# Kernel tuning notes

Measured on AMD Instinct MI355X. Metric: run time of the kernel, lower is better.

## Reference

```python
import jax, jax.numpy as jnp
import numpy as np

N = 50000      # nodes
E = 800000     # edges
F_IN = 512     # num_features
H = 128        # hidden


def setup_inputs() -> dict:
    key = jax.random.key(0)
    ks = jax.random.split(key, 10)
    edge_index = jax.random.randint(ks[0], (2, E), 0, N, dtype=jnp.int64 if jax.config.jax_enable_x64 else jnp.int32)
    x = jax.random.normal(ks[1], (N, F_IN), jnp.float32)
    weights = jax.random.uniform(ks[2], (E,), jnp.float32)
    def w(i, shape, fan):
        return jax.random.normal(ks[i], shape, jnp.float32) / np.sqrt(fan).astype(np.float32)
    return {
        "edge_index": edge_index,
        "x": x,
        "weights": weights,
        "W_lin1": w(3, (F_IN, H), F_IN), "b_lin1": jnp.zeros((H,), jnp.float32),
        "W_conv1": w(4, (H, 2 * H), H), "b_conv1": jnp.zeros((2 * H,), jnp.float32),
        "W_mu": w(5, (2 * H, H), 2 * H), "b_mu": jnp.zeros((H,), jnp.float32),
        "W_lin": w(6, (2 * H, 1), 2 * H), "b_lin": jnp.zeros((1,), jnp.float32),
    }


def gcn_conv(x, W, b, src, dst, ew, n):
    """PyG GCNConv with edge weights: add self-loops (weight 1), symmetric norm, scatter-add."""
    loop = jnp.arange(n, dtype=src.dtype)
    s2 = jnp.concatenate([src, loop])
    d2 = jnp.concatenate([dst, loop])
    w2 = jnp.concatenate([ew, jnp.ones((n,), x.dtype)])
    deg = jax.ops.segment_sum(w2, d2, num_segments=n)          # weighted in-degree incl. self-loop
    dinv = jnp.where(deg > 0, deg, 1.0) ** -0.5
    dinv = jnp.where(deg > 0, dinv, 0.0)
    norm = dinv[s2] * w2 * dinv[d2]                            # [E+N]
    h = x @ W                                                   # [N, out]
    out = jax.ops.segment_sum(h[s2] * norm[:, None], d2, num_segments=n)
    return out + b


def reference(edge_index, x, weights, W_lin1, b_lin1, W_conv1, b_conv1, W_mu, b_mu, W_lin, b_lin):
    n = x.shape[0]
    src, dst = edge_index[0], edge_index[1]
    # eval mode: dropout is identity, VGAE.encode returns mu
    h = x @ W_lin1 + b_lin1                                     # lin1
    h = jax.nn.relu(gcn_conv(h, W_conv1, b_conv1, src, dst, weights, n))
    z = gcn_conv(h, W_mu, b_mu, src, dst, weights, n)           # mu == embeddings
    emb_edges = jnp.concatenate([z[src], z[dst]], axis=1)       # [E, 2H]
    out = jax.nn.sigmoid(emb_edges @ W_lin + b_lin)
    return out.squeeze(-1)                                      # [E]
```

## Files before the change

### kernel.cpp

```cpp
#include <hip/hip_runtime.h>
#include <hip/hip_bf16.h>
#include <math.h>


#define NSL 256
#define RSH 8
#define RNG 256

typedef __attribute__((ext_vector_type(8))) short bf16x8;
typedef __attribute__((ext_vector_type(4))) float f32x4;

typedef const __attribute__((address_space(1))) unsigned int* gas_t;
typedef __attribute__((address_space(3))) unsigned int* las_t;

static __device__ __forceinline__ void gload_lds16(const void* g, void* l) {
    __builtin_amdgcn_global_load_lds((gas_t)g, (las_t)l, 16, 0, 0);
}

static __device__ __forceinline__ ushort f2b(float f) {
    __hip_bfloat16 h = __float2bfloat16(f);
    return *(ushort*)&h;
}
static __device__ __forceinline__ float b2f(ushort u) {
    unsigned int v = ((unsigned int)u) << 16;
    return *(float*)&v;
}
static __device__ __forceinline__ bf16x8 cvt8(float4 a, float4 b) {
    bf16x8 r;
    r[0] = (short)f2b(a.x); r[1] = (short)f2b(a.y); r[2] = (short)f2b(a.z); r[3] = (short)f2b(a.w);
    r[4] = (short)f2b(b.x); r[5] = (short)f2b(b.y); r[6] = (short)f2b(b.z); r[7] = (short)f2b(b.w);
    return r;
}


__global__ __launch_bounds__(256) void bucket_count(const int* __restrict__ dst,
                                                    int* __restrict__ cntA, int E, int NR) {
    __shared__ int lc[256];
    const int b = blockIdx.x, t = threadIdx.x;
    lc[t] = 0;
    __syncthreads();
    const int beg = (int)((long long)b * E / NSL);
    const int end = (int)((long long)(b + 1) * E / NSL);
    for (int e = beg + t; e < end; e += 256) atomicAdd(&lc[dst[e] >> RSH], 1);
    __syncthreads();
    if (t < NR) cntA[b * NR + t] = lc[t];
}

__global__ __launch_bounds__(256) void range_scan(int* __restrict__ cntA,
                                                  int* __restrict__ rtot, int NR) {
    __shared__ int s_[256];
    const int r = blockIdx.x, t = threadIdx.x;
    int v = cntA[t * NR + r];
    s_[t] = v;
    __syncthreads();
    for (int off = 1; off < 256; off <<= 1) {
        int add = (t >= off) ? s_[t - off] : 0;
        __syncthreads();
        s_[t] += add;
        __syncthreads();
    }
    cntA[t * NR + r] = s_[t] - v;
    if (t == 255) rtot[r] = s_[t];
}

__global__ __launch_bounds__(256) void base_scan(const int* __restrict__ rtot,
                                                 int* __restrict__ baseOut, int NR) {
    __shared__ int s_[256];
    const int t = threadIdx.x;
    int v = (t < NR) ? rtot[t] : 0;
    s_[t] = v;
    __syncthreads();
    for (int off = 1; off < 256; off <<= 1) {
        int add = (t >= off) ? s_[t - off] : 0;
        __syncthreads();
        s_[t] += add;
        __syncthreads();
    }
    if (t < NR) baseOut[t] = s_[t] - v;
    if (t == NR - 1) baseOut[NR] = s_[t];
}

__global__ __launch_bounds__(256) void bucket_scatter(const int* __restrict__ src,
                                                      const int* __restrict__ dst,
                                                      const float* __restrict__ w,
                                                      const int* __restrict__ cntA,
                                                      const int* __restrict__ baseOut,
                                                      uint2* __restrict__ rec, int E, int NR) {
    __shared__ int cur[256];
    const int b = blockIdx.x, t = threadIdx.x;
    if (t < NR) cur[t] = cntA[b * NR + t] + baseOut[t];
    __syncthreads();
    const int beg = (int)((long long)b * E / NSL);
    const int end = (int)((long long)(b + 1) * E / NSL);
    for (int e = beg + t; e < end; e += 256) {
        int d = dst[e];
        int r = d >> RSH;
        int pos = atomicAdd(&cur[r], 1);
        rec[pos] = make_uint2(((unsigned int)(d & (RNG - 1)) << 24) | (unsigned int)src[e],
                              __float_as_uint(w[e]));
    }
}

__global__ __launch_bounds__(256) void range_build(const uint2* __restrict__ rec,
                                                   const int* __restrict__ baseOut,
                                                   float* __restrict__ dinv,
                                                   int* __restrict__ offs,
                                                   uint2* __restrict__ ce,
                                                   int N, int E) {
    __shared__ float lw[256];
    __shared__ int lc[256];
    __shared__ int sc[256];
    const int r = blockIdx.x, t = threadIdx.x;
    lw[t] = 0.f; lc[t] = 0;
    __syncthreads();
    const int beg = baseOut[r], end = baseOut[r + 1];
    for (int e = beg + t; e < end; e += 256) {
        uint2 pk = rec[e];
        int dl = pk.x >> 24;
        atomicAdd(&lc[dl], 1);
        atomicAdd(&lw[dl], __uint_as_float(pk.y));
    }
    __syncthreads();
    int v = lc[t];
    sc[t] = v;
    __syncthreads();
    for (int off = 1; off < 256; off <<= 1) {
        int add = (t >= off) ? sc[t - off] : 0;
        __syncthreads();
        sc[t] += add;
        __syncthreads();
    }
    const int node = (r << RSH) + t;
    const int o = beg + sc[t] - v;
    if (node < N) {
        dinv[node] = 1.0f / sqrtf(1.0f + lw[t]);
        offs[node] = o;
    }
    if (r == 0 && t == 0) offs[N] = E;
    lc[t] = o;
    __syncthreads();
    for (int e = beg + t; e < end; e += 256) {
        uint2 pk = rec[e];
        int dl = pk.x >> 24;
        int pos = atomicAdd(&lc[dl], 1);
        ce[pos] = make_uint2(pk.x & 0xFFFFFF, pk.y);
    }
}


__global__ __launch_bounds__(256) void tconv_kernel(const float* __restrict__ B,
                                                    ushort* __restrict__ BT, int K, int Nn) {
    int i = blockIdx.x * 256 + threadIdx.x;
    if (i < K * Nn) {
        int k = i / Nn, n = i % Nn;
        BT[(size_t)n * K + k] = f2b(B[i]);
    }
}

__global__ __launch_bounds__(256) void fold_kernel(const float* __restrict__ Wm,
                                                   const float* __restrict__ Wl,
                                                   const float* __restrict__ bm,
                                                   float* __restrict__ wmp,
                                                   float* __restrict__ wmq,
                                                   float* __restrict__ bpq) {
    int j = threadIdx.x;
    float sp = 0.f, sq = 0.f;
    for (int k = 0; k < 128; ++k) {
        float v = Wm[(size_t)j * 128 + k];
        sp += v * Wl[k];
        sq += v * Wl[128 + k];
    }
    wmp[j] = sp; wmq[j] = sq;
    if (j == 0) { float s = 0.f; for (int k = 0; k < 128; ++k) s += bm[k] * Wl[k];       bpq[0] = s; }
    if (j == 1) { float s = 0.f; for (int k = 0; k < 128; ++k) s += bm[k] * Wl[128 + k]; bpq[1] = s; }
}

__global__ __launch_bounds__(256) void gemm1_mfma(const float* __restrict__ A,
                                                  const ushort* __restrict__ BT,
                                                  const float* __restrict__ bias,
                                                  const float* __restrict__ dinv,
                                                  ushort* __restrict__ C, int M) {
    __shared__ float  As[2][64 * 64];
    __shared__ ushort Bs[2][128 * 64];
    const int t = threadIdx.x;
    const int bm = blockIdx.x * 64;
    const int lane = t & 63;
    const int wid = t >> 6;
    const int wm = (wid >> 1) * 32, wn = (wid & 1) * 64;

    f32x4 acc[2][4] = {};

    const int a_row_l = (lane >> 4);
    const int a_ib    = (lane & 15) * 16;
    const int b_row_l = (lane >> 3);
    const int b_ib    = (lane & 7) * 16;

    auto stage = [&](int buf, int k0) {
#pragma unroll
        for (int j = 0; j < 4; ++j) {
            int c = wid * 4 + j;
            int row = c * 4 + a_row_l;
            int sw = a_ib ^ ((row & 7) << 5);
            int grow = min(bm + row, M - 1);
            const char* src = (const char*)A + ((size_t)grow * 512 + k0) * 4 + sw;
            gload_lds16(src, (char*)As[buf] + c * 1024);
        }
#pragma unroll
        for (int j = 0; j < 4; ++j) {
            int c = wid * 4 + j;
            int row = c * 8 + b_row_l;
            int sw = b_ib ^ ((row & 7) << 4);
            const char* src = (const char*)BT + (size_t)row * 1024 + k0 * 2 + sw;
            gload_lds16(src, (char*)Bs[buf] + c * 1024);
        }
    };

    stage(0, 0);
    int cur = 0;
#pragma unroll 1
    for (int tt = 0; tt < 8; ++tt) {
        if (tt < 7) {
            stage(cur ^ 1, (tt + 1) * 64);
            asm volatile("s_waitcnt vmcnt(8)" ::: "memory");
        } else {
            asm volatile("s_waitcnt vmcnt(0)" ::: "memory");
        }
        __builtin_amdgcn_sched_barrier(0);
        __builtin_amdgcn_s_barrier();
        const char* AsB = (const char*)As[cur];
        const char* BsB = (const char*)Bs[cur];
#pragma unroll
        for (int ks = 0; ks < 2; ++ks) {
            bf16x8 af[2], bfr[4];
#pragma unroll
            for (int mi = 0; mi < 2; ++mi) {
                int r = wm + mi * 16 + (lane & 15);
                int byte = r * 256 + ks * 128 + (lane >> 4) * 32;
                byte ^= (r & 7) << 5;
                float4 f0 = *(const float4*)(AsB + byte);
                float4 f1 = *(const float4*)(AsB + byte + 16);
                af[mi] = cvt8(f0, f1);
            }
#pragma unroll
            for (int ni = 0; ni < 4; ++ni) {
                int r = wn + ni * 16 + (lane & 15);
                int byte = r * 128 + ks * 64 + (lane >> 4) * 16;
                byte ^= (r & 7) << 4;
                bfr[ni] = *(const bf16x8*)(BsB + byte);
            }
#pragma unroll
            for (int mi = 0; mi < 2; ++mi)
#pragma unroll
                for (int ni = 0; ni < 4; ++ni)
                    acc[mi][ni] = __builtin_amdgcn_mfma_f32_16x16x32_bf16(af[mi], bfr[ni], acc[mi][ni], 0, 0, 0);
        }
        __builtin_amdgcn_s_barrier();
        cur ^= 1;
    }

#pragma unroll
    for (int mi = 0; mi < 2; ++mi)
#pragma unroll
        for (int r = 0; r < 4; ++r) {
            int row = bm + wm + mi * 16 + (lane >> 4) * 4 + r;
            if (row < M) {
                float dv = dinv[row];
#pragma unroll
                for (int ni = 0; ni < 4; ++ni) {
                    int col = wn + ni * 16 + (lane & 15);
                    C[(size_t)row * 128 + col] = f2b((acc[mi][ni][r] + bias[col]) * dv);
                }
            }
        }
}

__global__ __launch_bounds__(256) void aggregate_bf16(const ushort* __restrict__ hs,
                                                      const int* __restrict__ offs,
                                                      const uint2* __restrict__ ce,
                                                      const float* __restrict__ dinv,
                                                      ushort* __restrict__ out, int n) {
    int node = (int)((blockIdx.x * (size_t)blockDim.x + threadIdx.x) >> 6);
    int lane = threadIdx.x & 63;
    if (node >= n) return;
    unsigned int hv = *(const unsigned int*)(hs + (size_t)node * 128 + lane * 2);
    float ax = b2f((ushort)(hv & 0xffff));
    float ay = b2f((ushort)(hv >> 16));
    int beg = offs[node], end = offs[node + 1];
    for (int e = beg; e < end; e += 8) {
        uint2 rr[8];
#pragma unroll
        for (int j = 0; j < 8; ++j) {
            bool v = (e + j) < end;
            rr[j] = v ? ce[e + j] : make_uint2((unsigned)node, 0u);
        }
        unsigned int vv[8];
#pragma unroll
        for (int j = 0; j < 8; ++j)
            vv[j] = *(const unsigned int*)(hs + (size_t)rr[j].x * 128 + lane * 2);
#pragma unroll
        for (int j = 0; j < 8; ++j) {
            float wj = __uint_as_float(rr[j].y);
            ax += wj * b2f((ushort)(vv[j] & 0xffff));
            ay += wj * b2f((ushort)(vv[j] >> 16));
        }
    }
    float dv = dinv[node];
    unsigned int o = (unsigned int)f2b(ax * dv) | ((unsigned int)f2b(ay * dv) << 16);
    *(unsigned int*)(out + (size_t)node * 128 + lane * 2) = o;
}

__global__ __launch_bounds__(64) void gemm2_stream(const ushort* __restrict__ A,
                                                   const ushort* __restrict__ BT,
                                                   const float* __restrict__ bc,
                                                   const float* __restrict__ wmp,
                                                   const float* __restrict__ wmq,
                                                   const float* __restrict__ dinv,
                                                   float* __restrict__ pe,
                                                   float* __restrict__ qe, int M) {
    const int lane = threadIdx.x;
    const int r0 = blockIdx.x * 16;
    const int lrow = lane & 15;
    const int lk   = (lane >> 4) * 8;

    f32x4 acc[16] = {};

    const ushort* a  = A  + (size_t)min(r0 + lrow, M - 1) * 128 + lk;
    const ushort* bp = BT + (size_t)lrow * 128 + lk;

#pragma unroll
    for (int ks = 0; ks < 4; ++ks) {
        const int k0 = ks * 32;
        bf16x8 af = *(const bf16x8*)(a + k0);
#pragma unroll
        for (int ni = 0; ni < 16; ++ni) {
            bf16x8 bfr = *(const bf16x8*)(bp + (size_t)ni * 16 * 128 + k0);
            acc[ni] = __builtin_amdgcn_mfma_f32_16x16x32_bf16(af, bfr, acc[ni], 0, 0, 0);
        }
    }

    float bcv[16], wpv[16], wqv[16];
#pragma unroll
    for (int ni = 0; ni < 16; ++ni) {
        int col = ni * 16 + lrow;
        bcv[ni] = bc[col];
        wpv[ni] = wmp[col];
        wqv[ni] = wmq[col];
    }
#pragma unroll
    for (int r = 0; r < 4; ++r) {
        float sp = 0.f, sq = 0.f;
#pragma unroll
        for (int ni = 0; ni < 16; ++ni) {
            float h = fmaxf(acc[ni][r] + bcv[ni], 0.f);
            sp += h * wpv[ni];
            sq += h * wqv[ni];
        }
#pragma unroll
        for (int off = 1; off < 16; off <<= 1) {
            sp += __shfl_xor(sp, off);
            sq += __shfl_xor(sq, off);
        }
        if (lrow == 0) {
            int row = r0 + (lane >> 4) * 4 + r;
            if (row < M) {
                float dv = dinv[row];
                pe[row] = sp * dv;
                qe[row] = sq * dv;
            }
        }
    }
}

__global__ __launch_bounds__(256) void agg_scalar(const float* __restrict__ pe,
                                                  const float* __restrict__ qe,
                                                  const int* __restrict__ offs,
                                                  const uint2* __restrict__ ce,
                                                  const float* __restrict__ dinv,
                                                  const float* __restrict__ bpq,
                                                  float* __restrict__ p,
                                                  float* __restrict__ q, int n) {
    int i = blockIdx.x * 256 + threadIdx.x;
    if (i >= n) return;
    float ap = pe[i], aq = qe[i];
    int beg = offs[i], end = offs[i + 1];
    for (int k = beg; k < end; k += 4) {
        uint2 rr[4];
#pragma unroll
        for (int j = 0; j < 4; ++j) {
            bool v = (k + j) < end;
            rr[j] = v ? ce[k + j] : make_uint2((unsigned)i, 0u);
        }
        float pv[4], qv[4];
#pragma unroll
        for (int j = 0; j < 4; ++j) { pv[j] = pe[rr[j].x]; qv[j] = qe[rr[j].x]; }
#pragma unroll
        for (int j = 0; j < 4; ++j) {
            float wj = __uint_as_float(rr[j].y);
            ap += wj * pv[j];
            aq += wj * qv[j];
        }
    }
    float dv = dinv[i];
    p[i] = ap * dv + bpq[0];
    q[i] = aq * dv + bpq[1];
}

__global__ __launch_bounds__(256) void edge_out_kernel(const int* __restrict__ src,
                                                       const int* __restrict__ dst,
                                                       const float* __restrict__ p,
                                                       const float* __restrict__ q,
                                                       const float* __restrict__ bl,
                                                       float* __restrict__ out, int e) {
    int i = blockIdx.x * 256 + threadIdx.x;
    if (i < e) {
        float t = p[src[i]] + q[dst[i]] + bl[0];
        out[i] = 1.0f / (1.0f + expf(-t));
    }
}


extern "C" void kernel_launch(void* const* d_in, const int* in_sizes, int n_in,
                              void* d_out, int out_size, void* d_ws, size_t ws_size,
                              hipStream_t stream) {
    const int*   edge_index = (const int*)d_in[0];
    const float* x   = (const float*)d_in[1];
    const float* w   = (const float*)d_in[2];
    const float* W1  = (const float*)d_in[3];
    const float* b1  = (const float*)d_in[4];
    const float* Wc  = (const float*)d_in[5];
    const float* bc  = (const float*)d_in[6];
    const float* Wm  = (const float*)d_in[7];
    const float* bm  = (const float*)d_in[8];
    const float* Wl  = (const float*)d_in[9];
    const float* bl  = (const float*)d_in[10];
    float* out = (float*)d_out;

    const int E  = in_sizes[2];
    const int H  = in_sizes[4];
    const int F  = in_sizes[3] / H;
    const int N  = in_sizes[1] / F;
    const int H2 = 2 * H;
    const int NR = (N + RNG - 1) / RNG;

    const int* src = edge_index;
    const int* dst = edge_index + E;

    char* ws = (char*)d_ws;
    size_t off = 0;
    auto alloc = [&](size_t bytes) -> void* {
        off = (off + 255) & ~(size_t)255;
        void* r = ws + off;
        off += bytes;
        return r;
    };
    int*    cntA    = (int*)   alloc((size_t)NSL * NR * 4);
    int*    rtot    = (int*)   alloc((size_t)NR * 4);
    int*    baseOut = (int*)   alloc((size_t)(NR + 1) * 4);
    uint2*  rec     = (uint2*) alloc((size_t)E * 8);
    uint2*  ce      = (uint2*) alloc((size_t)E * 8);
    float*  dinv    = (float*) alloc((size_t)N * 4);
    int*    offs    = (int*)   alloc((size_t)(N + 1) * 4);
    ushort* hs_bf   = (ushort*)alloc((size_t)N * H * 2);
    ushort* agg1_bf = (ushort*)alloc((size_t)N * H * 2);
    ushort* W1T     = (ushort*)alloc((size_t)H * F * 2);
    ushort* WcT     = (ushort*)alloc((size_t)H2 * H * 2);
    float*  wmp     = (float*) alloc(H2 * 4);
    float*  wmq     = (float*) alloc(H2 * 4);
    float*  bpq     = (float*) alloc(2 * 4);
    float*  pe      = (float*) alloc((size_t)N * 4);
    float*  qe      = (float*) alloc((size_t)N * 4);
    float*  p       = (float*) alloc((size_t)N * 4);
    float*  q       = (float*) alloc((size_t)N * 4);
    (void)ws_size; (void)n_in; (void)out_size;

    int nbN  = (N + 255) / 256;
    int nbE  = (E + 255) / 256;
    int nbW  = (int)(((size_t)N * 64 + 255) / 256);
    int nb64 = (N + 63) / 64;
    int nb16 = (N + 15) / 16;

    bucket_count<<<NSL, 256, 0, stream>>>(dst, cntA, E, NR);
    range_scan<<<NR, 256, 0, stream>>>(cntA, rtot, NR);
    base_scan<<<1, 256, 0, stream>>>(rtot, baseOut, NR);
    bucket_scatter<<<NSL, 256, 0, stream>>>(src, dst, w, cntA, baseOut, rec, E, NR);
    range_build<<<NR, 256, 0, stream>>>(rec, baseOut, dinv, offs, ce, N, E);

    tconv_kernel<<<(F * H + 255) / 256, 256, 0, stream>>>(W1, W1T, F, H);
    tconv_kernel<<<(H * H2 + 255) / 256, 256, 0, stream>>>(Wc, WcT, H, H2);
    fold_kernel<<<1, 256, 0, stream>>>(Wm, Wl, bm, wmp, wmq, bpq);

    gemm1_mfma<<<nb64, 256, 0, stream>>>(x, W1T, b1, dinv, hs_bf, N);
    aggregate_bf16<<<nbW, 256, 0, stream>>>(hs_bf, offs, ce, dinv, agg1_bf, N);
    gemm2_stream<<<nb16, 64, 0, stream>>>(agg1_bf, WcT, bc, wmp, wmq, dinv, pe, qe, N);
    agg_scalar<<<nbN, 256, 0, stream>>>(pe, qe, offs, ce, dinv, bpq, p, q, N);
    edge_out_kernel<<<nbE, 256, 0, stream>>>(src, dst, p, q, bl, out, E);
}
```

Before: 197.7 us.

## Merge weight prep kernels into one launch and single-buffer gemm1 LDS

Three small prep kernels (two weight transposes to bf16 and the Wm/Wl fold) become one launch that picks its job from the block index, saving two kernel launches. Separately, gemm1 drops its LDS double-buffering: each k-step now loads a tile, syncs, computes and syncs again. This halves gemm1's shared memory, which may let more blocks share a CU, but global loads no longer overlap MFMA work.

```diff
diff --git a/kernel.cpp b/kernel.cpp
--- a/kernel.cpp
+++ b/kernel.cpp
@@ -147,32 +147,43 @@
     }
 }
 
-
-__global__ __launch_bounds__(256) void tconv_kernel(const float* __restrict__ B,
-                                                    ushort* __restrict__ BT, int K, int Nn) {
-    int i = blockIdx.x * 256 + threadIdx.x;
-    if (i < K * Nn) {
-        int k = i / Nn, n = i % Nn;
-        BT[(size_t)n * K + k] = f2b(B[i]);
-    }
-}
-
-__global__ __launch_bounds__(256) void fold_kernel(const float* __restrict__ Wm,
+__global__ __launch_bounds__(256) void prep_kernel(const float* __restrict__ W1,
+                                                   const float* __restrict__ Wc,
+                                                   const float* __restrict__ Wm,
                                                    const float* __restrict__ Wl,
                                                    const float* __restrict__ bm,
+                                                   ushort* __restrict__ W1T,
+                                                   ushort* __restrict__ WcT,
                                                    float* __restrict__ wmp,
                                                    float* __restrict__ wmq,
-                                                   float* __restrict__ bpq) {
-    int j = threadIdx.x;
-    float sp = 0.f, sq = 0.f;
-    for (int k = 0; k < 128; ++k) {
-        float v = Wm[(size_t)j * 128 + k];
-        sp += v * Wl[k];
-        sq += v * Wl[128 + k];
-    }
-    wmp[j] = sp; wmq[j] = sq;
-    if (j == 0) { float s = 0.f; for (int k = 0; k < 128; ++k) s += bm[k] * Wl[k];       bpq[0] = s; }
-    if (j == 1) { float s = 0.f; for (int k = 0; k < 128; ++k) s += bm[k] * Wl[128 + k]; bpq[1] = s; }
+                                                   float* __restrict__ bpq,
+                                                   int F, int H, int H2,
+                                                   int nb1, int nb2) {
+    const int b = blockIdx.x, t = threadIdx.x;
+    if (b < nb1) {
+        int i = b * 256 + t;
+        if (i < F * H) {
+            int k = i / H, n = i % H;
+            W1T[(size_t)n * F + k] = f2b(W1[i]);
+        }
+    } else if (b < nb1 + nb2) {
+        int i = (b - nb1) * 256 + t;
+        if (i < H * H2) {
+            int k = i / H2, n = i % H2;
+            WcT[(size_t)n * H + k] = f2b(Wc[i]);
+        }
+    } else {
+        int j = t;
+        float sp = 0.f, sq = 0.f;
+        for (int k = 0; k < 128; ++k) {
+            float v = Wm[(size_t)j * 128 + k];
+            sp += v * Wl[k];
+            sq += v * Wl[128 + k];
+        }
+        wmp[j] = sp; wmq[j] = sq;
+        if (j == 0) { float s = 0.f; for (int k = 0; k < 128; ++k) s += bm[k] * Wl[k];       bpq[0] = s; }
+        if (j == 1) { float s = 0.f; for (int k = 0; k < 128; ++k) s += bm[k] * Wl[128 + k]; bpq[1] = s; }
+    }
 }
 
 __global__ __launch_bounds__(256) void gemm1_mfma(const float* __restrict__ A,
@@ -180,8 +191,10 @@
                                                   const float* __restrict__ bias,
                                                   const float* __restrict__ dinv,
                                                   ushort* __restrict__ C, int M) {
-    __shared__ float  As[2][64 * 64];
-    __shared__ ushort Bs[2][128 * 64];
+    __shared__ float  As[64 * 64];
+    __shared__ ushort Bs[128 * 64];
+    char* AsB = (char*)As;
+    char* BsB = (char*)Bs;
     const int t = threadIdx.x;
     const int bm = blockIdx.x * 64;
     const int lane = t & 63;
@@ -195,7 +208,9 @@
     const int b_row_l = (lane >> 3);
     const int b_ib    = (lane & 7) * 16;
 
-    auto stage = [&](int buf, int k0) {
+#pragma unroll 1
+    for (int tt = 0; tt < 8; ++tt) {
+        const int k0 = tt * 64;
 #pragma unroll
         for (int j = 0; j < 4; ++j) {
             int c = wid * 4 + j;
@@ -203,7 +218,7 @@
             int sw = a_ib ^ ((row & 7) << 5);
             int grow = min(bm + row, M - 1);
             const char* src = (const char*)A + ((size_t)grow * 512 + k0) * 4 + sw;
-            gload_lds16(src, (char*)As[buf] + c * 1024);
+            gload_lds16(src, AsB + c * 1024);
         }
 #pragma unroll
         for (int j = 0; j < 4; ++j) {
@@ -211,24 +226,9 @@
             int row = c * 8 + b_row_l;
             int sw = b_ib ^ ((row & 7) << 4);
             const char* src = (const char*)BT + (size_t)row * 1024 + k0 * 2 + sw;
-            gload_lds16(src, (char*)Bs[buf] + c * 1024);
-        }
-    };
-
-    stage(0, 0);
-    int cur = 0;
-#pragma unroll 1
-    for (int tt = 0; tt < 8; ++tt) {
-        if (tt < 7) {
-            stage(cur ^ 1, (tt + 1) * 64);
-            asm volatile("s_waitcnt vmcnt(8)" ::: "memory");
-        } else {
-            asm volatile("s_waitcnt vmcnt(0)" ::: "memory");
-        }
-        __builtin_amdgcn_sched_barrier(0);
-        __builtin_amdgcn_s_barrier();
-        const char* AsB = (const char*)As[cur];
-        const char* BsB = (const char*)Bs[cur];
+            gload_lds16(src, BsB + c * 1024);
+        }
+        __syncthreads();
 #pragma unroll
         for (int ks = 0; ks < 2; ++ks) {
             bf16x8 af[2], bfr[4];
@@ -254,8 +254,7 @@
                 for (int ni = 0; ni < 4; ++ni)
                     acc[mi][ni] = __builtin_amdgcn_mfma_f32_16x16x32_bf16(af[mi], bfr[ni], acc[mi][ni], 0, 0, 0);
         }
-        __builtin_amdgcn_s_barrier();
-        cur ^= 1;
+        __syncthreads();
     }
 
 #pragma unroll
@@ -478,6 +477,8 @@
     int nbW  = (int)(((size_t)N * 64 + 255) / 256);
     int nb64 = (N + 63) / 64;
     int nb16 = (N + 15) / 16;
+    int nb1  = (F * H + 255) / 256;
+    int nb2  = (H * H2 + 255) / 256;
 
     bucket_count<<<NSL, 256, 0, stream>>>(dst, cntA, E, NR);
     range_scan<<<NR, 256, 0, stream>>>(cntA, rtot, NR);
@@ -485,9 +486,8 @@
     bucket_scatter<<<NSL, 256, 0, stream>>>(src, dst, w, cntA, baseOut, rec, E, NR);
     range_build<<<NR, 256, 0, stream>>>(rec, baseOut, dinv, offs, ce, N, E);
 
-    tconv_kernel<<<(F * H + 255) / 256, 256, 0, stream>>>(W1, W1T, F, H);
-    tconv_kernel<<<(H * H2 + 255) / 256, 256, 0, stream>>>(Wc, WcT, H, H2);
-    fold_kernel<<<1, 256, 0, stream>>>(Wm, Wl, bm, wmp, wmq, bpq);
+    prep_kernel<<<nb1 + nb2 + 1, 256, 0, stream>>>(W1, Wc, Wm, Wl, bm, W1T, WcT,
+                                                   wmp, wmq, bpq, F, H, H2, nb1, nb2);
 
     gemm1_mfma<<<nb64, 256, 0, stream>>>(x, W1T, b1, dinv, hs_bf, N);
     aggregate_bf16<<<nbW, 256, 0, stream>>>(hs_bf, offs, ce, dinv, agg1_bf, N);
```

Result: faster. 190.0 us (-3.9%).
